# Kernel optimization log

Measured on AMD Instinct MI355X. Metric: run time of the kernel, lower is better.

## Reference

```python
import jax, jax.numpy as jnp
import numpy as np

D_MODEL, H, D_K, D_V, D_FF = 1024, 16, 64, 64, 4096
B, L = 2, 2048
EPS = 1e-5


def layer_norm(x, g, b):
    mu = jnp.mean(x, axis=-1, keepdims=True)
    var = jnp.mean(jnp.square(x - mu), axis=-1, keepdims=True)
    return (x - mu) * jax.lax.rsqrt(var + EPS) * g + b


def setup_inputs() -> dict:
    key = jax.random.key(0)
    ks = jax.random.split(key, 12)
    s = 0.02
    x = jax.random.normal(ks[0], (B, L, D_MODEL), dtype=jnp.float32)
    Wq = jax.random.normal(ks[1], (H, D_MODEL, D_K), dtype=jnp.float32) * s
    Wk = jax.random.normal(ks[2], (H, D_MODEL, D_K), dtype=jnp.float32) * s
    Wv = jax.random.normal(ks[3], (H, D_MODEL, D_V), dtype=jnp.float32) * s
    bq = jnp.zeros((H, D_K), dtype=jnp.float32)
    bk = jnp.zeros((H, D_K), dtype=jnp.float32)
    bv = jnp.zeros((H, D_V), dtype=jnp.float32)
    Wo = jax.random.normal(ks[4], (H * D_V, D_MODEL), dtype=jnp.float32) * s
    W1 = jax.random.normal(ks[5], (D_MODEL, D_FF), dtype=jnp.float32) * s
    b1 = jnp.zeros((D_FF,), dtype=jnp.float32)
    W2 = jax.random.normal(ks[6], (D_FF, D_MODEL), dtype=jnp.float32) * s
    ln1_g = jnp.ones((D_MODEL,), dtype=jnp.float32)
    ln1_b = jnp.zeros((D_MODEL,), dtype=jnp.float32)
    ln2_g = jnp.ones((D_MODEL,), dtype=jnp.float32)
    ln2_b = jnp.zeros((D_MODEL,), dtype=jnp.float32)
    return dict(x=x, Wq=Wq, bq=bq, Wk=Wk, bk=bk, Wv=Wv, bv=bv, Wo=Wo,
                ln1_g=ln1_g, ln1_b=ln1_b, W1=W1, b1=b1, W2=W2,
                ln2_g=ln2_g, ln2_b=ln2_b)


def reference(x, Wq, bq, Wk, bk, Wv, bv, Wo, ln1_g, ln1_b, W1, b1, W2, ln2_g, ln2_b):
    # Batched multi-head attention (all heads at once, equivalent to the
    # per-head Python loop in the original module).
    Q = jnp.einsum('bld,hdk->bhlk', x, Wq) + bq[None, :, None, :]
    K = jnp.einsum('bld,hdk->bhlk', x, Wk) + bk[None, :, None, :]
    V = jnp.einsum('bld,hdv->bhlv', x, Wv) + bv[None, :, None, :]
    scores = jnp.einsum('bhlk,bhmk->bhlm', Q, K) * (1.0 / jnp.sqrt(jnp.float32(D_K)))
    attn = jax.nn.softmax(scores, axis=-1)
    O = jnp.einsum('bhlm,bhmv->bhlv', attn, V)        # [b,h,l,dv]
    O = jnp.transpose(O, (0, 2, 1, 3)).reshape(x.shape[0], x.shape[1], H * D_V)
    mha = O @ Wo                                       # [b,l,d_model]
    # residual + LayerNorm (dropout_prob=0 -> identity)
    h1 = layer_norm(x + mha, ln1_g, ln1_b)
    ff = jax.nn.relu(h1 @ W1 + b1) @ W2
    return layer_norm(h1 + ff, ln2_g, ln2_b)
```

## Files before the change

kernel.cpp:

```cpp
#include <hip/hip_runtime.h>

typedef unsigned short u16;
typedef unsigned int u32;
typedef short bf16x8 __attribute__((ext_vector_type(8)));
typedef float f32x4 __attribute__((ext_vector_type(4)));
typedef unsigned int u32x2 __attribute__((ext_vector_type(2)));
typedef unsigned int u32x4 __attribute__((ext_vector_type(4)));

#define D_MODEL 1024
#define NH 16
#define DK 64
#define DFF 4096
#define BATCH 2
#define SEQ 2048
#define BL (BATCH*SEQ)
#define NQKV 3072
#define Q_SCALE 0.18033688011f

__device__ __forceinline__ float bfraw2f(u16 u) {
    union { u32 i; float f; } c; c.i = ((u32)u) << 16; return c.f;
}
__device__ __forceinline__ u16 f2bfraw(float f) {
    union { float f; u32 i; } c; c.f = f;
    u32 i = c.i;
    u32 lsb = (i >> 16) & 1u;
    i += 0x7fffu + lsb;
    return (u16)(i >> 16);
}
__device__ __forceinline__ u32 fasu(float f) {
    union { float f; u32 i; } c; c.f = f; return c.i;
}
__device__ __forceinline__ u32 pack_bf2(float lo, float hi) {
    return __builtin_amdgcn_perm(fasu(hi) + 0x8000u, fasu(lo) + 0x8000u,
                                 0x07060302u);
}
__device__ __forceinline__ void gload_lds16(const u16* g, u16* l) {
    __builtin_amdgcn_global_load_lds(
        (const __attribute__((address_space(1))) void*)g,
        (__attribute__((address_space(3))) void*)l, 16, 0, 0);
}

__global__ __launch_bounds__(256) void cast_f32_bf16(const float* __restrict__ in,
                                                     u16* __restrict__ out) {
    int i = (blockIdx.x * 256 + threadIdx.x) * 4;
    f32x4 v = *(const f32x4*)&in[i];
#pragma unroll
    for (int j = 0; j < 4; j++) out[i + j] = f2bfraw(v[j]);
}

__global__ __launch_bounds__(256) void prep_weights(
    const float* __restrict__ Wq, const float* __restrict__ Wk,
    const float* __restrict__ Wv, const float* __restrict__ Wo,
    const float* __restrict__ W1, const float* __restrict__ W2,
    const float* __restrict__ bq, const float* __restrict__ bk,
    const float* __restrict__ bv,
    u16* __restrict__ wqkv_t, u16* __restrict__ wo_t,
    u16* __restrict__ w1_t, u16* __restrict__ w2_t,
    float* __restrict__ bqkv) {
    __shared__ u16 t[64][65];
    const int z = blockIdx.z, bx = blockIdx.x;
    const int col = threadIdx.x & 63, rr = threadIdx.x >> 6;

    if (z < 3) {
        if (bx >= 256) {
            if (z == 0 && bx < 268) {
                int i = (bx - 256) * 256 + threadIdx.x;
                bqkv[i] = (i < 1024) ? bq[i]
                        : (i < 2048) ? bk[i - 1024] : bv[i - 2048];
            }
            return;
        }
        const int d0 = (bx & 15) * 64, h = bx >> 4;
        const float* W = (z == 0) ? Wq : (z == 1) ? Wk : Wv;
        const float* src = W + (size_t)h * D_MODEL * DK;
        for (int i = rr; i < 64; i += 4)
            t[i][col] = f2bfraw(src[(size_t)(d0 + i) * DK + col]);
        __syncthreads();
        u16* dst = wqkv_t + (size_t)(z * 1024 + h * 64) * D_MODEL;
        for (int i = rr; i < 64; i += 4)
            dst[(size_t)i * D_MODEL + d0 + col] = t[col][i];
        return;
    }

    const float* in; u16* out; int R, C;
    if (z == 3)      { in = Wo; out = wo_t; R = 1024; C = 1024; }
    else if (z == 4) { in = W1; out = w1_t; R = 1024; C = 4096; }
    else             { in = W2; out = w2_t; R = 4096; C = 1024; }
    const int ctiles = C >> 6;
    const int rt = bx / ctiles, ct = bx % ctiles;
    if (rt >= (R >> 6)) return;
    const int c0 = ct * 64, r0 = rt * 64;
    for (int i = rr; i < 64; i += 4)
        t[i][col] = f2bfraw(in[(size_t)(r0 + i) * C + c0 + col]);
    __syncthreads();
    for (int i = rr; i < 64; i += 4)
        out[(size_t)(c0 + i) * R + r0 + col] = t[col][i];
}


template <int OUT_F32, int RELU, int HASBIAS, int SPLITK, int SCALEQ, int VSTORE>
__global__ __launch_bounds__(256, 4) void gemm_bt(const u16* __restrict__ A,
                                                  const u16* __restrict__ Bt,
                                                  const float* __restrict__ bias,
                                                  void* __restrict__ Cout,
                                                  u16* __restrict__ vtout,
                                                  int M, int N, int K) {
    __shared__ __attribute__((aligned(16))) u16 As[128 * 64];
    __shared__ __attribute__((aligned(16))) u16 Bs[128 * 64];
    const int tid = threadIdx.x;
    const int lane = tid & 63, wid = tid >> 6;
    const int quad = lane >> 4, l16 = lane & 15;
    const int m0 = blockIdx.x * 128, n0 = blockIdx.y * 128;
    const int z = (SPLITK > 1) ? blockIdx.z : 0;
    const int Klen = K / SPLITK;
    const int kend = (z + 1) * Klen;
    const int wm = (wid >> 1) * 64, wn = (wid & 1) * 64;

    f32x4 acc[4][4];
#pragma unroll
    for (int i = 0; i < 4; i++)
#pragma unroll
        for (int j = 0; j < 4; j++) acc[i][j] = (f32x4){0.f, 0.f, 0.f, 0.f};

    const int srow = lane >> 3, scol = (lane & 7) * 8;

    for (int kb = z * Klen; kb < kend; kb += 64) {
#pragma unroll
        for (int p = 0; p < 4; p++) {
            int c = wid * 4 + p;
            int row = c * 8 + srow;
            gload_lds16(&A[(size_t)(m0 + row) * K + kb + scol], &As[c * 512]);
            gload_lds16(&Bt[(size_t)(n0 + row) * K + kb + scol], &Bs[c * 512]);
        }
        __syncthreads();
#pragma unroll
        for (int kh = 0; kh < 2; kh++) {
            bf16x8 af[4], bf[4];
#pragma unroll
            for (int t = 0; t < 4; t++) {
                af[t] = *(const bf16x8*)&As[(wm + t * 16 + l16) * 64 + kh * 32 + quad * 8];
                bf[t] = *(const bf16x8*)&Bs[(wn + t * 16 + l16) * 64 + kh * 32 + quad * 8];
            }
#pragma unroll
            for (int i = 0; i < 4; i++)
#pragma unroll
                for (int j = 0; j < 4; j++)
                    acc[i][j] = __builtin_amdgcn_mfma_f32_16x16x32_bf16(
                        af[i], bf[j], acc[i][j], 0, 0, 0);
        }
        __syncthreads();
    }

    if (VSTORE && n0 >= 2048) {
#pragma unroll
        for (int i = 0; i < 4; i++) {
            int row0 = m0 + wm + i * 16 + quad * 4;
            int bb = row0 >> 11, l = row0 & 2047;
#pragma unroll
            for (int j = 0; j < 4; j++) {
                int col = n0 + wn + j * 16 + l16;
                float bv = HASBIAS ? bias[col] : 0.f;
                int dv = col - 2048;
                u32x2 w;
                w.x = pack_bf2(acc[i][j][0] + bv, acc[i][j][1] + bv);
                w.y = pack_bf2(acc[i][j][2] + bv, acc[i][j][3] + bv);
                *(u32x2*)&vtout[((size_t)(bb * 1024 + dv)) * 2048 + l] = w;
            }
        }
        return;
    }

    float* outf = (float*)Cout + (size_t)z * M * N;
#pragma unroll
    for (int i = 0; i < 4; i++) {
#pragma unroll
        for (int j = 0; j < 4; j++) {
#pragma unroll
            for (int r = 0; r < 4; r++) {
                int row = m0 + wm + i * 16 + quad * 4 + r;
                int col = n0 + wn + j * 16 + l16;
                float v = acc[i][j][r];
                if (HASBIAS) v += bias[col];
                if (RELU) v = v > 0.f ? v : 0.f;
                if (SCALEQ && col < 1024) v *= Q_SCALE;
                if (OUT_F32)
                    outf[(size_t)row * N + col] = v;
                else
                    ((u16*)Cout)[(size_t)row * N + col] = f2bfraw(v);
            }
        }
    }
}

__global__ __launch_bounds__(512, 4) void attn_kernel(const u16* __restrict__ qkv,
                                                      const u16* __restrict__ vt,
                                                      u16* __restrict__ O) {
    __shared__ __attribute__((aligned(16))) u16 Ks[2][128 * 64];
    __shared__ __attribute__((aligned(16))) u16 Vs[64 * 128];

    const int tid = threadIdx.x;
    const int lane = tid & 63, wid = tid >> 6;
    const int quad = lane >> 4, l16 = lane & 15;
    const int sw = l16 & 7;
    const int b = blockIdx.z, h = blockIdx.y;
    const int q0 = blockIdx.x * 128 + wid * 16;

    const size_t qrow = (size_t)(b * SEQ + q0 + l16) * NQKV + h * DK;
    const bf16x8 qf0 = *(const bf16x8*)&qkv[qrow + quad * 8];
    const bf16x8 qf1 = *(const bf16x8*)&qkv[qrow + 32 + quad * 8];

    const u16* Kbase = qkv + (size_t)(b * SEQ) * NQKV + D_MODEL + h * DK;
    const u16* Vbase = vt + (size_t)((b * NH + h) * DK) * SEQ;

    f32x4 oacc[4];
#pragma unroll
    for (int d = 0; d < 4; d++) oacc[d] = (f32x4){0.f, 0.f, 0.f, 0.f};
    float lr = 0.f;
    const f32x4 Z = {0.f, 0.f, 0.f, 0.f};

    auto stage_k = [&](int kt2, int buf) {
#pragma unroll
        for (int p = 0; p < 2; p++) {
            int seg = p * 8 + wid;
            int row = seg * 8 + (lane >> 3);
            int chunk = (lane & 7) ^ (lane >> 3);
            gload_lds16(&Kbase[(size_t)(kt2 + row) * NQKV + chunk * 8],
                        &Ks[buf][seg * 512]);
        }
    };
    bf16x8 vreg[2];
    auto load_v = [&](int kt2) {
#pragma unroll
        for (int p = 0; p < 2; p++) {
            int s = p * 512 + tid;
            vreg[p] = *(const bf16x8*)&Vbase[(size_t)(s >> 4) * SEQ + kt2 + (s & 15) * 8];
        }
    };
    stage_k(0, 0);
    load_v(0);

    for (int t = 0; t < SEQ / 128; t++) {
        const int kt = t * 128;
#pragma unroll
        for (int p = 0; p < 2; p++) {
            int s = p * 512 + tid;
            int vr = s >> 4, vc = s & 15;
            int chunkA = (vc >> 2) * 4 + (vc & 1) * 2;
            int rem = ((vc >> 1) & 1) * 4;
            u32x4 kv = __builtin_bit_cast(u32x4, vreg[p]);
            *(u32x2*)&Vs[vr * 128 + ((chunkA ^ (vr & 7)) * 8) + rem] =
                (u32x2){kv.x, kv.y};
            *(u32x2*)&Vs[vr * 128 + (((chunkA + 1) ^ (vr & 7)) * 8) + rem] =
                (u32x2){kv.z, kv.w};
        }
        __syncthreads();

        if (t + 1 < SEQ / 128) {
            stage_k(kt + 128, (t + 1) & 1);
            load_v(kt + 128);
        }

        const u16* kb = Ks[t & 1];

        f32x4 sacc[8];
        __builtin_amdgcn_s_setprio(1);
#pragma unroll
        for (int nt = 0; nt < 8; nt++) {
            const u16* krow = &kb[(nt * 16 + l16) * 64];
            bf16x8 kf0 = *(const bf16x8*)&krow[(quad ^ sw) * 8];
            bf16x8 kf1 = *(const bf16x8*)&krow[((4 + quad) ^ sw) * 8];
            f32x4 s0 = __builtin_amdgcn_mfma_f32_16x16x32_bf16(kf0, qf0, Z, 0, 0, 0);
            sacc[nt] = __builtin_amdgcn_mfma_f32_16x16x32_bf16(kf1, qf1, s0, 0, 0, 0);
        }
        __builtin_amdgcn_s_setprio(0);

        u32 wreg[8][2];
#pragma unroll
        for (int nt = 0; nt < 8; nt++) {
            float p0 = __builtin_amdgcn_exp2f(sacc[nt][0]);
            float p1 = __builtin_amdgcn_exp2f(sacc[nt][1]);
            float p2 = __builtin_amdgcn_exp2f(sacc[nt][2]);
            float p3 = __builtin_amdgcn_exp2f(sacc[nt][3]);
            lr += (p0 + p1) + (p2 + p3);
            wreg[nt][0] = pack_bf2(p0, p1);
            wreg[nt][1] = pack_bf2(p2, p3);
        }

        __builtin_amdgcn_s_setprio(1);
#pragma unroll
        for (int ks = 0; ks < 4; ks++) {
            u32x4 pw = (u32x4){wreg[2 * ks][0], wreg[2 * ks][1],
                               wreg[2 * ks + 1][0], wreg[2 * ks + 1][1]};
            bf16x8 pf = __builtin_bit_cast(bf16x8, pw);
#pragma unroll
            for (int d = 0; d < 4; d++) {
                bf16x8 vf = *(const bf16x8*)&Vs[(d * 16 + l16) * 128 +
                                                (((ks * 4 + quad) ^ sw) * 8)];
                oacc[d] = __builtin_amdgcn_mfma_f32_16x16x32_bf16(vf, pf, oacc[d], 0, 0, 0);
            }
        }
        __builtin_amdgcn_s_setprio(0);
        __syncthreads();
    }

    lr += __shfl_xor(lr, 16, 64);
    lr += __shfl_xor(lr, 32, 64);
    float iv = 1.f / lr;

    size_t row = (size_t)(b * SEQ + q0 + l16);
#pragma unroll
    for (int d = 0; d < 4; d++) {
        float o0 = oacc[d][0] * iv, o1 = oacc[d][1] * iv;
        float o2 = oacc[d][2] * iv, o3 = oacc[d][3] * iv;
        u32x2 w;
        w.x = ((u32)f2bfraw(o1) << 16) | f2bfraw(o0);
        w.y = ((u32)f2bfraw(o3) << 16) | f2bfraw(o2);
        *(u32x2*)&O[row * D_MODEL + h * DK + d * 16 + quad * 4] = w;
    }
}

__global__ __launch_bounds__(256) void ln3_kernel(const float* __restrict__ xa,
                                                  const float* __restrict__ xb,
                                                  const float* __restrict__ xc,
                                                  const float* __restrict__ g,
                                                  const float* __restrict__ be,
                                                  u16* __restrict__ out_bf,
                                                  float* __restrict__ out_f) {
    int row = blockIdx.x;
    int tid = threadIdx.x;
    const float* pa = xa + (size_t)row * D_MODEL;
    const float* pb = xb + (size_t)row * D_MODEL;
    const float* pc = xc + (size_t)row * D_MODEL;
    int c = tid * 4;
    f32x4 av = *(const f32x4*)&pa[c];
    f32x4 bv = *(const f32x4*)&pb[c];
    f32x4 cv = *(const f32x4*)&pc[c];
    float v[4];
    float s = 0.f, ss = 0.f;
#pragma unroll
    for (int i = 0; i < 4; i++) {
        v[i] = av[i] + bv[i] + cv[i];
        s += v[i];
        ss += v[i] * v[i];
    }
#pragma unroll
    for (int off = 32; off; off >>= 1) {
        s += __shfl_down(s, off, 64);
        ss += __shfl_down(ss, off, 64);
    }
    __shared__ float red[8];
    int wid = tid >> 6, lane = tid & 63;
    if (lane == 0) { red[wid] = s; red[4 + wid] = ss; }
    __syncthreads();
    if (tid == 0) {
        red[0] = red[0] + red[1] + red[2] + red[3];
        red[4] = red[4] + red[5] + red[6] + red[7];
    }
    __syncthreads();
    float mu = red[0] * (1.f / D_MODEL);
    float var = red[4] * (1.f / D_MODEL) - mu * mu;
    float rs = rsqrtf(var + 1e-5f);
#pragma unroll
    for (int i = 0; i < 4; i++) {
        float o = (v[i] - mu) * rs * g[c + i] + be[c + i];
        if (out_f) out_f[(size_t)row * D_MODEL + c + i] = o;
        if (out_bf) out_bf[(size_t)row * D_MODEL + c + i] = f2bfraw(o);
    }
}

extern "C" void kernel_launch(void* const* d_in, const int* in_sizes, int n_in,
                              void* d_out, int out_size, void* d_ws, size_t ws_size,
                              hipStream_t stream) {
    const float* x   = (const float*)d_in[0];
    const float* Wq  = (const float*)d_in[1];
    const float* bq  = (const float*)d_in[2];
    const float* Wk  = (const float*)d_in[3];
    const float* bk  = (const float*)d_in[4];
    const float* Wv  = (const float*)d_in[5];
    const float* bv  = (const float*)d_in[6];
    const float* Wo  = (const float*)d_in[7];
    const float* g1  = (const float*)d_in[8];
    const float* be1 = (const float*)d_in[9];
    const float* W1  = (const float*)d_in[10];
    const float* b1  = (const float*)d_in[11];
    const float* W2  = (const float*)d_in[12];
    const float* g2  = (const float*)d_in[13];
    const float* be2 = (const float*)d_in[14];

    char* w = (char*)d_ws;
    auto alloc = [&](size_t bytes) {
        char* p = w;
        w += (bytes + 255) & ~(size_t)255;
        return p;
    };
    u16* wqkv_t = (u16*)alloc((size_t)NQKV * D_MODEL * 2);
    u16* wo_t   = (u16*)alloc((size_t)D_MODEL * D_MODEL * 2);
    u16* w1_t   = (u16*)alloc((size_t)DFF * D_MODEL * 2);
    u16* w2_t   = (u16*)alloc((size_t)D_MODEL * DFF * 2);
    float* bqkv = (float*)alloc((size_t)NQKV * 4);
    u16* x_bf   = (u16*)alloc((size_t)BL * D_MODEL * 2);
    u16* qkvbuf = (u16*)alloc((size_t)BL * NQKV * 2);
    u16* vtbuf  = (u16*)alloc((size_t)BATCH * NH * DK * SEQ * 2);
    u16* obuf   = (u16*)alloc((size_t)BL * D_MODEL * 2);
    float* mha_p = (float*)alloc((size_t)2 * BL * D_MODEL * 4);
    u16* h1_bf  = (u16*)alloc((size_t)BL * D_MODEL * 2);
    float* h1_f = (float*)alloc((size_t)BL * D_MODEL * 4);
    u16* ffa    = (u16*)alloc((size_t)BL * DFF * 2);
    float* ffb_p = (float*)alloc((size_t)2 * BL * D_MODEL * 4);

    cast_f32_bf16<<<dim3(BL * D_MODEL / 1024), 256, 0, stream>>>(x, x_bf);
    prep_weights<<<dim3(1024, 1, 6), 256, 0, stream>>>(
        Wq, Wk, Wv, Wo, W1, W2, bq, bk, bv, wqkv_t, wo_t, w1_t, w2_t, bqkv);

    gemm_bt<0, 0, 1, 1, 1, 1><<<dim3(32, 24), 256, 0, stream>>>(
        x_bf, wqkv_t, bqkv, qkvbuf, vtbuf, BL, NQKV, D_MODEL);
    attn_kernel<<<dim3(16, 16, 2), 512, 0, stream>>>(qkvbuf, vtbuf, obuf);
    gemm_bt<1, 0, 0, 2, 0, 0><<<dim3(32, 8, 2), 256, 0, stream>>>(
        obuf, wo_t, nullptr, mha_p, nullptr, BL, D_MODEL, D_MODEL);
    ln3_kernel<<<dim3(BL), 256, 0, stream>>>(x, mha_p, mha_p + (size_t)BL * D_MODEL,
                                             g1, be1, h1_bf, h1_f);
    gemm_bt<0, 1, 1, 1, 0, 0><<<dim3(32, 32), 256, 0, stream>>>(
        h1_bf, w1_t, b1, ffa, nullptr, BL, DFF, D_MODEL);
    gemm_bt<1, 0, 0, 2, 0, 0><<<dim3(32, 8, 2), 256, 0, stream>>>(
        ffa, w2_t, nullptr, ffb_p, nullptr, BL, D_MODEL, DFF);
    ln3_kernel<<<dim3(BL), 256, 0, stream>>>(h1_f, ffb_p, ffb_p + (size_t)BL * D_MODEL,
                                             g2, be2, nullptr, (float*)d_out);
}
```

Measured before the change: 359.0 us.

## Process two query tiles per wave in attention and fold x cast into prep

The attention kernel now runs 4 waves of 256 threads, each handling 32 query rows as two 16-row tiles. Each K fragment and V fragment read from LDS then feeds two MFMAs, which halves LDS traffic per unit of compute. The cost is more accumulator and score registers and fewer waves to hide latency. Separately, the x fp32-to-bf16 cast moves into a seventh z-slice of the weight-prep kernel, removing one kernel launch.

```diff
diff --git a/kernel.cpp b/kernel.cpp
--- a/kernel.cpp
+++ b/kernel.cpp
@@ -40,26 +40,29 @@
         (__attribute__((address_space(3))) void*)l, 16, 0, 0);
 }
 
-__global__ __launch_bounds__(256) void cast_f32_bf16(const float* __restrict__ in,
-                                                     u16* __restrict__ out) {
-    int i = (blockIdx.x * 256 + threadIdx.x) * 4;
-    f32x4 v = *(const f32x4*)&in[i];
-#pragma unroll
-    for (int j = 0; j < 4; j++) out[i + j] = f2bfraw(v[j]);
-}
-
 __global__ __launch_bounds__(256) void prep_weights(
     const float* __restrict__ Wq, const float* __restrict__ Wk,
     const float* __restrict__ Wv, const float* __restrict__ Wo,
     const float* __restrict__ W1, const float* __restrict__ W2,
     const float* __restrict__ bq, const float* __restrict__ bk,
-    const float* __restrict__ bv,
+    const float* __restrict__ bv, const float* __restrict__ x,
     u16* __restrict__ wqkv_t, u16* __restrict__ wo_t,
     u16* __restrict__ w1_t, u16* __restrict__ w2_t,
-    float* __restrict__ bqkv) {
+    float* __restrict__ bqkv, u16* __restrict__ x_bf) {
     __shared__ u16 t[64][65];
     const int z = blockIdx.z, bx = blockIdx.x;
     const int col = threadIdx.x & 63, rr = threadIdx.x >> 6;
+
+    if (z == 6) {
+#pragma unroll
+        for (int j = 0; j < 4; j++) {
+            int i = (((j << 10) + bx) * 256 + threadIdx.x) * 4;
+            f32x4 v = *(const f32x4*)&x[i];
+#pragma unroll
+            for (int e = 0; e < 4; e++) x_bf[i + e] = f2bfraw(v[e]);
+        }
+        return;
+    }
 
     if (z < 3) {
         if (bx >= 256) {
@@ -192,7 +195,7 @@
     }
 }
 
-__global__ __launch_bounds__(512, 4) void attn_kernel(const u16* __restrict__ qkv,
+__global__ __launch_bounds__(256, 2) void attn_kernel(const u16* __restrict__ qkv,
                                                       const u16* __restrict__ vt,
                                                       u16* __restrict__ O) {
     __shared__ __attribute__((aligned(16))) u16 Ks[2][128 * 64];
@@ -203,36 +206,43 @@
     const int quad = lane >> 4, l16 = lane & 15;
     const int sw = l16 & 7;
     const int b = blockIdx.z, h = blockIdx.y;
-    const int q0 = blockIdx.x * 128 + wid * 16;
-
-    const size_t qrow = (size_t)(b * SEQ + q0 + l16) * NQKV + h * DK;
-    const bf16x8 qf0 = *(const bf16x8*)&qkv[qrow + quad * 8];
-    const bf16x8 qf1 = *(const bf16x8*)&qkv[qrow + 32 + quad * 8];
+    const int q0 = blockIdx.x * 128 + wid * 32;
+
+    bf16x8 qf[2][2];
+#pragma unroll
+    for (int qt = 0; qt < 2; qt++) {
+        const size_t qrow = (size_t)(b * SEQ + q0 + qt * 16 + l16) * NQKV + h * DK;
+        qf[qt][0] = *(const bf16x8*)&qkv[qrow + quad * 8];
+        qf[qt][1] = *(const bf16x8*)&qkv[qrow + 32 + quad * 8];
+    }
 
     const u16* Kbase = qkv + (size_t)(b * SEQ) * NQKV + D_MODEL + h * DK;
     const u16* Vbase = vt + (size_t)((b * NH + h) * DK) * SEQ;
 
-    f32x4 oacc[4];
-#pragma unroll
-    for (int d = 0; d < 4; d++) oacc[d] = (f32x4){0.f, 0.f, 0.f, 0.f};
-    float lr = 0.f;
+    f32x4 oacc[4][2];
+#pragma unroll
+    for (int d = 0; d < 4; d++) {
+        oacc[d][0] = (f32x4){0.f, 0.f, 0.f, 0.f};
+        oacc[d][1] = (f32x4){0.f, 0.f, 0.f, 0.f};
+    }
+    float lr[2] = {0.f, 0.f};
     const f32x4 Z = {0.f, 0.f, 0.f, 0.f};
 
     auto stage_k = [&](int kt2, int buf) {
 #pragma unroll
-        for (int p = 0; p < 2; p++) {
-            int seg = p * 8 + wid;
-            int row = seg * 8 + (lane >> 3);
+        for (int p = 0; p < 4; p++) {
+            int g = p * 4 + wid;
+            int row = g * 8 + (lane >> 3);
             int chunk = (lane & 7) ^ (lane >> 3);
             gload_lds16(&Kbase[(size_t)(kt2 + row) * NQKV + chunk * 8],
-                        &Ks[buf][seg * 512]);
+                        &Ks[buf][g * 512]);
         }
     };
-    bf16x8 vreg[2];
+    bf16x8 vreg[4];
     auto load_v = [&](int kt2) {
 #pragma unroll
-        for (int p = 0; p < 2; p++) {
-            int s = p * 512 + tid;
+        for (int p = 0; p < 4; p++) {
+            int s = p * 256 + tid;
             vreg[p] = *(const bf16x8*)&Vbase[(size_t)(s >> 4) * SEQ + kt2 + (s & 15) * 8];
         }
     };
@@ -242,8 +252,8 @@
     for (int t = 0; t < SEQ / 128; t++) {
         const int kt = t * 128;
 #pragma unroll
-        for (int p = 0; p < 2; p++) {
-            int s = p * 512 + tid;
+        for (int p = 0; p < 4; p++) {
+            int s = p * 256 + tid;
             int vr = s >> 4, vc = s & 15;
             int chunkA = (vc >> 2) * 4 + (vc & 1) * 2;
             int rem = ((vc >> 1) & 1) * 4;
@@ -262,60 +272,77 @@
 
         const u16* kb = Ks[t & 1];
 
-        f32x4 sacc[8];
+        f32x4 sacc[8][2];
         __builtin_amdgcn_s_setprio(1);
 #pragma unroll
         for (int nt = 0; nt < 8; nt++) {
             const u16* krow = &kb[(nt * 16 + l16) * 64];
             bf16x8 kf0 = *(const bf16x8*)&krow[(quad ^ sw) * 8];
             bf16x8 kf1 = *(const bf16x8*)&krow[((4 + quad) ^ sw) * 8];
-            f32x4 s0 = __builtin_amdgcn_mfma_f32_16x16x32_bf16(kf0, qf0, Z, 0, 0, 0);
-            sacc[nt] = __builtin_amdgcn_mfma_f32_16x16x32_bf16(kf1, qf1, s0, 0, 0, 0);
+#pragma unroll
+            for (int qt = 0; qt < 2; qt++) {
+                f32x4 s0 = __builtin_amdgcn_mfma_f32_16x16x32_bf16(kf0, qf[qt][0], Z, 0, 0, 0);
+                sacc[nt][qt] = __builtin_amdgcn_mfma_f32_16x16x32_bf16(kf1, qf[qt][1], s0, 0, 0, 0);
+            }
         }
         __builtin_amdgcn_s_setprio(0);
 
-        u32 wreg[8][2];
-#pragma unroll
-        for (int nt = 0; nt < 8; nt++) {
-            float p0 = __builtin_amdgcn_exp2f(sacc[nt][0]);
-            float p1 = __builtin_amdgcn_exp2f(sacc[nt][1]);
-            float p2 = __builtin_amdgcn_exp2f(sacc[nt][2]);
-            float p3 = __builtin_amdgcn_exp2f(sacc[nt][3]);
-            lr += (p0 + p1) + (p2 + p3);
-            wreg[nt][0] = pack_bf2(p0, p1);
-            wreg[nt][1] = pack_bf2(p2, p3);
+        u32 wreg[2][8][2];
+#pragma unroll
+        for (int qt = 0; qt < 2; qt++) {
+#pragma unroll
+            for (int nt = 0; nt < 8; nt++) {
+                float p0 = __builtin_amdgcn_exp2f(sacc[nt][qt][0]);
+                float p1 = __builtin_amdgcn_exp2f(sacc[nt][qt][1]);
+                float p2 = __builtin_amdgcn_exp2f(sacc[nt][qt][2]);
+                float p3 = __builtin_amdgcn_exp2f(sacc[nt][qt][3]);
+                lr[qt] += (p0 + p1) + (p2 + p3);
+                wreg[qt][nt][0] = pack_bf2(p0, p1);
+                wreg[qt][nt][1] = pack_bf2(p2, p3);
+            }
         }
 
         __builtin_amdgcn_s_setprio(1);
 #pragma unroll
         for (int ks = 0; ks < 4; ks++) {
-            u32x4 pw = (u32x4){wreg[2 * ks][0], wreg[2 * ks][1],
-                               wreg[2 * ks + 1][0], wreg[2 * ks + 1][1]};
-            bf16x8 pf = __builtin_bit_cast(bf16x8, pw);
+            bf16x8 pf[2];
+#pragma unroll
+            for (int qt = 0; qt < 2; qt++) {
+                u32x4 pw = (u32x4){wreg[qt][2 * ks][0], wreg[qt][2 * ks][1],
+                                   wreg[qt][2 * ks + 1][0], wreg[qt][2 * ks + 1][1]};
+                pf[qt] = __builtin_bit_cast(bf16x8, pw);
+            }
 #pragma unroll
             for (int d = 0; d < 4; d++) {
                 bf16x8 vf = *(const bf16x8*)&Vs[(d * 16 + l16) * 128 +
                                                 (((ks * 4 + quad) ^ sw) * 8)];
-                oacc[d] = __builtin_amdgcn_mfma_f32_16x16x32_bf16(vf, pf, oacc[d], 0, 0, 0);
+                oacc[d][0] = __builtin_amdgcn_mfma_f32_16x16x32_bf16(vf, pf[0], oacc[d][0], 0, 0, 0);
+                oacc[d][1] = __builtin_amdgcn_mfma_f32_16x16x32_bf16(vf, pf[1], oacc[d][1], 0, 0, 0);
             }
         }
         __builtin_amdgcn_s_setprio(0);
         __syncthreads();
     }
 
-    lr += __shfl_xor(lr, 16, 64);
-    lr += __shfl_xor(lr, 32, 64);
-    float iv = 1.f / lr;
-
-    size_t row = (size_t)(b * SEQ + q0 + l16);
-#pragma unroll
-    for (int d = 0; d < 4; d++) {
-        float o0 = oacc[d][0] * iv, o1 = oacc[d][1] * iv;
-        float o2 = oacc[d][2] * iv, o3 = oacc[d][3] * iv;
-        u32x2 w;
-        w.x = ((u32)f2bfraw(o1) << 16) | f2bfraw(o0);
-        w.y = ((u32)f2bfraw(o3) << 16) | f2bfraw(o2);
-        *(u32x2*)&O[row * D_MODEL + h * DK + d * 16 + quad * 4] = w;
+#pragma unroll
+    for (int qt = 0; qt < 2; qt++) {
+        lr[qt] += __shfl_xor(lr[qt], 16, 64);
+        lr[qt] += __shfl_xor(lr[qt], 32, 64);
+    }
+
+#pragma unroll
+    for (int qt = 0; qt < 2; qt++) {
+        float iv = 1.f / lr[qt];
+        size_t row = (size_t)(b * SEQ + q0 + qt * 16 + l16);
+#pragma unroll
+        for (int d = 0; d < 4; d++) {
+            float o0 = oacc[d][qt][0] * iv, o1 = oacc[d][qt][1] * iv;
+            float o2 = oacc[d][qt][2] * iv, o3 = oacc[d][qt][3] * iv;
+            u32x2 w;
+            w.x = ((u32)f2bfraw(o1) << 16) | f2bfraw(o0);
+            w.y = ((u32)f2bfraw(o3) << 16) | f2bfraw(o2);
+            *(u32x2*)&O[row * D_MODEL + h * DK + d * 16 + quad * 4] = w;
+        }
     }
 }
 
@@ -408,13 +435,13 @@
     u16* ffa    = (u16*)alloc((size_t)BL * DFF * 2);
     float* ffb_p = (float*)alloc((size_t)2 * BL * D_MODEL * 4);
 
-    cast_f32_bf16<<<dim3(BL * D_MODEL / 1024), 256, 0, stream>>>(x, x_bf);
-    prep_weights<<<dim3(1024, 1, 6), 256, 0, stream>>>(
-        Wq, Wk, Wv, Wo, W1, W2, bq, bk, bv, wqkv_t, wo_t, w1_t, w2_t, bqkv);
+    prep_weights<<<dim3(1024, 1, 7), 256, 0, stream>>>(
+        Wq, Wk, Wv, Wo, W1, W2, bq, bk, bv, x,
+        wqkv_t, wo_t, w1_t, w2_t, bqkv, x_bf);
 
     gemm_bt<0, 0, 1, 1, 1, 1><<<dim3(32, 24), 256, 0, stream>>>(
         x_bf, wqkv_t, bqkv, qkvbuf, vtbuf, BL, NQKV, D_MODEL);
-    attn_kernel<<<dim3(16, 16, 2), 512, 0, stream>>>(qkvbuf, vtbuf, obuf);
+    attn_kernel<<<dim3(16, 16, 2), 256, 0, stream>>>(qkvbuf, vtbuf, obuf);
     gemm_bt<1, 0, 0, 2, 0, 0><<<dim3(32, 8, 2), 256, 0, stream>>>(
         obuf, wo_t, nullptr, mha_p, nullptr, BL, D_MODEL, D_MODEL);
     ln3_kernel<<<dim3(BL), 256, 0, stream>>>(x, mha_p, mha_p + (size_t)BL * D_MODEL,
```

Result: slower. 367.1 us (+2.3%).
